# Optimization experiments

Hardware: AMD Instinct MI355X
Metric: run time of the kernel (lower is better)

## Reference

```python
import jax, jax.numpy as jnp
import numpy as np

# Config (matches BlockConfig defaults for linear attention)
B, S, D = 2, 4096, 2048
H, KVH, HD, CK = 16, 8, 128, 4   # n_heads, n_kv_heads, head_dim, conv_kernel
DQK, DV = KVH * HD, H * HD       # 1024, 2048
EPS = 1e-6


def setup_inputs() -> dict:
    key = jax.random.key(0)
    ks = jax.random.split(key, 12)
    std = 0.02
    return {
        "x": jax.random.normal(ks[0], (B, S, D), jnp.float32),
        "wq": jax.random.normal(ks[1], (DQK, D), jnp.float32) * std,
        "wk": jax.random.normal(ks[2], (DQK, D), jnp.float32) * std,
        "wv": jax.random.normal(ks[3], (DV, D), jnp.float32) * std,
        "wo": jax.random.normal(ks[4], (D, DV), jnp.float32) * std,
        "q_conv_w": jax.random.normal(ks[5], (DQK, 1, CK), jnp.float32) * std,
        "k_conv_w": jax.random.normal(ks[6], (DQK, 1, CK), jnp.float32) * std,
        "alpha_w": jax.random.normal(ks[7], (H, D), jnp.float32) * std,
        "alpha_b": jnp.zeros((H,), jnp.float32),
        "beta_w": jax.random.normal(ks[8], (H, D), jnp.float32) * std,
        "beta_b": jnp.zeros((H,), jnp.float32),
        "g_w": jax.random.normal(ks[9], (DV, D), jnp.float32) * std,
        "norm_q_w": jnp.ones((HD,), jnp.float32),
        "norm_k_w": jnp.ones((HD,), jnp.float32),
    }


def _rmsnorm(x, w):
    # normalize over last dim (head_dim) in fp32, elementwise affine, no bias
    xf = x.astype(jnp.float32)
    var = jnp.mean(xf * xf, axis=-1, keepdims=True)
    return (w * xf * jax.lax.rsqrt(var + EPS)).astype(x.dtype)


def _causal_dwconv(x, w):
    # x: (B, S, C); w: (C, 1, k) depthwise; torch Conv1d padding=k-1 then [:S]
    # == left-pad (k-1, 0) cross-correlation
    y = jax.lax.conv_general_dilated(
        x.transpose(0, 2, 1), w, window_strides=(1,),
        padding=[(CK - 1, 0)], feature_group_count=w.shape[0],
        dimension_numbers=("NCH", "OIH", "NCH"))
    return y.transpose(0, 2, 1)


def reference(x, wq, wk, wv, wo, q_conv_w, k_conv_w,
              alpha_w, alpha_b, beta_w, beta_b, g_w, norm_q_w, norm_k_w):
    Q = x @ wq.T                              # (B,S,DQK)
    K = x @ wk.T                              # (B,S,DQK)
    V = x @ wv.T                              # (B,S,DV)
    Q = _causal_dwconv(Q, q_conv_w)
    K = _causal_dwconv(K, k_conv_w)
    Q = _rmsnorm(Q.reshape(B, S, KVH, HD), norm_q_w)
    K = _rmsnorm(K.reshape(B, S, KVH, HD), norm_k_w)
    V = V.reshape(B, S, H, HD)
    alpha = jax.nn.sigmoid(x @ alpha_w.T + alpha_b)              # (B,S,H)
    beta = jax.nn.sigmoid(x @ beta_w.T + beta_b) / (HD ** 0.5)   # (B,S,H)
    rep = H // KVH
    Q = jnp.repeat(Q, rep, axis=2)            # (B,S,H,HD)
    K = jnp.repeat(K, rep, axis=2)

    # time-major for scan
    Qt = Q.transpose(1, 0, 2, 3)
    Kt = K.transpose(1, 0, 2, 3)
    Vt = V.transpose(1, 0, 2, 3)
    at = alpha.transpose(1, 0, 2)
    bt = beta.transpose(1, 0, 2)

    S0 = jnp.zeros((B, H, HD, HD), x.dtype)

    def step(S_state, inp):
        q_t, k_t, v_t, a_t, b_t = inp
        pred = jnp.einsum("bhd,bhdv->bhv", k_t, S_state)
        delta = v_t - pred
        update = jnp.einsum("bhv,bhd->bhdv", delta, k_t)
        S_state = a_t[:, :, None, None] * S_state + b_t[:, :, None, None] * update
        o_t = jnp.einsum("bhd,bhdv->bhv", q_t, S_state)
        return S_state, o_t

    _, O = jax.lax.scan(step, S0, (Qt, Kt, Vt, at, bt))  # O: (S,B,H,HD)
    out = O.transpose(1, 0, 2, 3).reshape(B, S, DV)
    g = jax.nn.sigmoid(x @ g_w.T)
    return (g * out) @ wo.T
```

## Files before the change

### kernel.cpp

```cpp
#include <hip/hip_runtime.h>
#include <stdint.h>

#define DEV static __device__ __forceinline__

typedef __bf16 bf16x8 __attribute__((ext_vector_type(8)));
typedef float f32x4 __attribute__((ext_vector_type(4)));

constexpr int Bc = 2, Sc = 4096, Dc = 2048, Hc = 16, KVHc = 8, HDc = 128;
constexpr int DQKc = 1024, DVc = 2048;
constexpr int Mc = Bc * Sc;
constexpr int NCATc = 6144;
constexpr int CT = 64;
constexpr int NCH = Sc / CT;
constexpr int COEF_STRIDE = 16896;
constexpr float EPSc = 1e-6f;

DEV uint16_t f2bf(float f) {
  uint32_t u = __float_as_uint(f);
  u += 0x7FFFu + ((u >> 16) & 1u);
  return (uint16_t)(u >> 16);
}
DEV float bf2f(uint16_t h) { return __uint_as_float(((uint32_t)h) << 16); }
DEV float sigmoidf_(float z) { return 1.0f / (1.0f + __expf(-z)); }

DEV void gload16(void* lds, const void* g) {
  auto gp = (const __attribute__((address_space(1))) uint32_t*)(uintptr_t)g;
  auto lp = (__attribute__((address_space(3))) uint32_t*)(uint32_t)(uintptr_t)lds;
  __builtin_amdgcn_global_load_lds(gp, lp, 16, 0, 0);
}

__global__ __launch_bounds__(256) void cast_kernel(const float* __restrict__ src,
                                                   uint16_t* __restrict__ dst, int n4) {
  int i = blockIdx.x * blockDim.x + threadIdx.x;
  int stride = gridDim.x * blockDim.x;
  for (; i < n4; i += stride) {
    float4 v = *(const float4*)(src + (size_t)i * 4);
    ushort4 o;
    o.x = f2bf(v.x); o.y = f2bf(v.y); o.z = f2bf(v.z); o.w = f2bf(v.w);
    *(ushort4*)(dst + (size_t)i * 4) = o;
  }
}

template <typename OutT>
__global__ __launch_bounds__(512, 2) void gemm256_bt(const uint16_t* __restrict__ A,
                                                     const uint16_t* __restrict__ Bw,
                                                     OutT* __restrict__ C, int Ndim, int Kdim,
                                                     int lda) {
  __shared__ uint16_t sT[2][2][2][8192];

  const int nbn = Ndim / 256;
  const int nwg = gridDim.x;
  int q = nwg >> 3, r = nwg & 7;
  int xcd = blockIdx.x & 7, lin = blockIdx.x >> 3;
  int swz = (xcd < r ? xcd * (q + 1) : r * (q + 1) + (xcd - r) * q) + lin;
  const int bm = swz / nbn, bn = swz % nbn;

  const int tid = threadIdx.x;
  const int wid = tid >> 6, lane = tid & 63;
  const int wm = wid >> 2, wn = wid & 3;
  const int lr = lane & 15;
  const int sswz8 = (((lane >> 4) ^ ((lr >> 1) & 3)) * 8);
  const int arow_base = wm * 128 + lr;
  const int brow_base = wn * 64 + lr;

  const uint16_t* Ab = A + (size_t)(bm * 256) * lda;
  const uint16_t* Bb = Bw + (size_t)(bn * 256) * Kdim;
  const int NT = Kdim >> 6;

  int srowA[2];
  int soff[2];
  const int wbase = tid & ~63;
#pragma unroll
  for (int u = 0; u < 2; ++u) {
    int L = u * 512 + tid;
    srowA[u] = L >> 2;
    soff[u] = (((L & 3) ^ ((L >> 3) & 3)) * 8);
  }

  auto STAGE = [&](int buf, int mat, int kh, int kt) {
    const uint16_t* gb = mat == 0 ? Ab : Bb;
    const int ld = mat == 0 ? lda : Kdim;
    uint16_t* rg = &sT[buf][mat][kh][0];
#pragma unroll
    for (int u = 0; u < 2; ++u) {
      const uint16_t* g = gb + (size_t)srowA[u] * ld + kt * 64 + kh * 32 + soff[u];
      gload16(rg + (u * 512 + wbase) * 8, g);
    }
  };

  f32x4 acc[8][4] = {};
  bf16x8 bfr[4];

  STAGE(0, 0, 0, 0); STAGE(0, 1, 0, 0);
  STAGE(0, 0, 1, 0); STAGE(0, 1, 1, 0);
  STAGE(1, 0, 0, 1); STAGE(1, 1, 0, 1);
  asm volatile("s_waitcnt vmcnt(4)" ::: "memory");
  __builtin_amdgcn_s_barrier();

  for (int kt = 0; kt < NT; ++kt) {
    const int buf = kt & 1;
    const uint16_t* aR0 = &sT[buf][0][0][0];
    const uint16_t* bR0 = &sT[buf][1][0][0];
    const uint16_t* aR1 = &sT[buf][0][1][0];
    const uint16_t* bR1 = &sT[buf][1][1][0];

    {
      bf16x8 af[4];
#pragma unroll
      for (int m = 0; m < 4; ++m)
        af[m] = *(const bf16x8*)&aR0[(arow_base + m * 16) * 32 + sswz8];
#pragma unroll
      for (int n = 0; n < 4; ++n)
        bfr[n] = *(const bf16x8*)&bR0[(brow_base + n * 16) * 32 + sswz8];
      if (kt + 1 < NT) STAGE(buf ^ 1, 0, 1, kt + 1);
      __builtin_amdgcn_s_setprio(1);
#pragma unroll
      for (int m = 0; m < 4; ++m)
#pragma unroll
        for (int n = 0; n < 4; ++n)
          acc[m][n] = __builtin_amdgcn_mfma_f32_16x16x32_bf16(af[m], bfr[n], acc[m][n], 0, 0, 0);
      __builtin_amdgcn_s_setprio(0);
      __builtin_amdgcn_s_barrier();
    }
    {
      bf16x8 af[4];
#pragma unroll
      for (int m = 0; m < 4; ++m)
        af[m] = *(const bf16x8*)&aR0[(arow_base + (m + 4) * 16) * 32 + sswz8];
      if (kt + 1 < NT) STAGE(buf ^ 1, 1, 1, kt + 1);
      __builtin_amdgcn_s_setprio(1);
#pragma unroll
      for (int m = 0; m < 4; ++m)
#pragma unroll
        for (int n = 0; n < 4; ++n)
          acc[m + 4][n] = __builtin_amdgcn_mfma_f32_16x16x32_bf16(af[m], bfr[n], acc[m + 4][n], 0, 0, 0);
      __builtin_amdgcn_s_setprio(0);
      __builtin_amdgcn_s_barrier();
    }
    {
      bf16x8 af[4];
#pragma unroll
      for (int m = 0; m < 4; ++m)
        af[m] = *(const bf16x8*)&aR1[(arow_base + m * 16) * 32 + sswz8];
#pragma unroll
      for (int n = 0; n < 4; ++n)
        bfr[n] = *(const bf16x8*)&bR1[(brow_base + n * 16) * 32 + sswz8];
      if (kt + 2 < NT) STAGE(buf, 0, 0, kt + 2);
      __builtin_amdgcn_s_setprio(1);
#pragma unroll
      for (int m = 0; m < 4; ++m)
#pragma unroll
        for (int n = 0; n < 4; ++n)
          acc[m][n] = __builtin_amdgcn_mfma_f32_16x16x32_bf16(af[m], bfr[n], acc[m][n], 0, 0, 0);
      __builtin_amdgcn_s_setprio(0);
      __builtin_amdgcn_s_barrier();
    }
    {
      bf16x8 af[4];
#pragma unroll
      for (int m = 0; m < 4; ++m)
        af[m] = *(const bf16x8*)&aR1[(arow_base + (m + 4) * 16) * 32 + sswz8];
      if (kt + 2 < NT) STAGE(buf, 1, 0, kt + 2);
      __builtin_amdgcn_s_setprio(1);
#pragma unroll
      for (int m = 0; m < 4; ++m)
#pragma unroll
        for (int n = 0; n < 4; ++n)
          acc[m + 4][n] = __builtin_amdgcn_mfma_f32_16x16x32_bf16(af[m], bfr[n], acc[m + 4][n], 0, 0, 0);
      __builtin_amdgcn_s_setprio(0);
    }
    if (kt + 1 < NT) {
      if (kt + 2 < NT)
        asm volatile("s_waitcnt vmcnt(4)" ::: "memory");
      else
        asm volatile("s_waitcnt vmcnt(0)" ::: "memory");
      __builtin_amdgcn_s_barrier();
    }
  }

  const int r0 = (lane >> 4) * 4;
#pragma unroll
  for (int m = 0; m < 8; ++m)
#pragma unroll
    for (int n = 0; n < 4; ++n) {
      int col = bn * 256 + wn * 64 + n * 16 + lr;
#pragma unroll
      for (int j = 0; j < 4; ++j) {
        int row = bm * 256 + wm * 128 + m * 16 + r0 + j;
        float val = acc[m][n][j];
        if constexpr (sizeof(OutT) == 2)
          C[(size_t)row * Ndim + col] = (OutT)f2bf(val);
        else
          C[(size_t)row * Ndim + col] = (OutT)val;
      }
    }
}

__global__ __launch_bounds__(256) void alphabeta_kernel(const float* __restrict__ x,
                                                        const float* __restrict__ aw,
                                                        const float* __restrict__ abias,
                                                        const float* __restrict__ bw,
                                                        const float* __restrict__ bbias,
                                                        float* __restrict__ out) {
  __shared__ float xs[4 * Dc];
  const int row0 = blockIdx.x * 4;
  const float* xp = x + (size_t)row0 * Dc;
  for (int i = threadIdx.x; i < 4 * Dc / 4; i += 256)
    *(float4*)&xs[i * 4] = *(const float4*)(xp + (size_t)i * 4);
  __syncthreads();
  const int o = threadIdx.x >> 3, lg = threadIdx.x & 7;
  const float* wrow = (o < 16) ? (aw + (size_t)o * Dc) : (bw + (size_t)(o - 16) * Dc);
  float s0 = 0.f, s1 = 0.f, s2 = 0.f, s3 = 0.f;
  for (int k = lg * 4; k < Dc; k += 32) {
    float4 wv = *(const float4*)(wrow + k);
    float4 x0 = *(const float4*)&xs[k];
    float4 x1 = *(const float4*)&xs[Dc + k];
    float4 x2 = *(const float4*)&xs[2 * Dc + k];
    float4 x3 = *(const float4*)&xs[3 * Dc + k];
    s0 += x0.x * wv.x + x0.y * wv.y + x0.z * wv.z + x0.w * wv.w;
    s1 += x1.x * wv.x + x1.y * wv.y + x1.z * wv.z + x1.w * wv.w;
    s2 += x2.x * wv.x + x2.y * wv.y + x2.z * wv.z + x2.w * wv.w;
    s3 += x3.x * wv.x + x3.y * wv.y + x3.z * wv.z + x3.w * wv.w;
  }
#pragma unroll
  for (int m = 1; m < 8; m <<= 1) {
    s0 += __shfl_xor(s0, m); s1 += __shfl_xor(s1, m);
    s2 += __shfl_xor(s2, m); s3 += __shfl_xor(s3, m);
  }
  if (lg == 0) {
    float bias = (o < 16) ? abias[o] : bbias[o - 16];
    float scale = (o >= 16) ? 0.08838834764831845f : 1.0f;
    out[(size_t)(row0 + 0) * 32 + o] = sigmoidf_(s0 + bias) * scale;
    out[(size_t)(row0 + 1) * 32 + o] = sigmoidf_(s1 + bias) * scale;
    out[(size_t)(row0 + 2) * 32 + o] = sigmoidf_(s2 + bias) * scale;
    out[(size_t)(row0 + 3) * 32 + o] = sigmoidf_(s3 + bias) * scale;
  }
}

__global__ __launch_bounds__(256) void convnorm_kernel(const uint16_t* __restrict__ C1,
                                                       const float* __restrict__ qcw,
                                                       const float* __restrict__ kcw,
                                                       const float* __restrict__ nqw,
                                                       const float* __restrict__ nkw,
                                                       uint16_t* __restrict__ Qn,
                                                       uint16_t* __restrict__ Kn) {
  const int wid = blockIdx.x * 4 + (threadIdx.x >> 6);
  const int lane = threadIdx.x & 63;
  const int kvh = wid & 7;
  const int t = (wid >> 3) & (Sc - 1);
  const int b = wid >> 15;
  float qv[2], kv[2];
#pragma unroll
  for (int half = 0; half < 2; ++half) {
    const int c = lane + half * 64;
    const int ch = kvh * HDc + c;
    float qs = 0.f, ks = 0.f;
#pragma unroll
    for (int j = 0; j < 4; ++j) {
      int tt = t - 3 + j;
      if (tt >= 0) {
        size_t rb = (size_t)(b * Sc + tt) * NCATc;
        qs = fmaf(bf2f(C1[rb + ch]), qcw[ch * 4 + j], qs);
        ks = fmaf(bf2f(C1[rb + 1024 + ch]), kcw[ch * 4 + j], ks);
      }
    }
    qv[half] = qs; kv[half] = ks;
  }
  float sq = qv[0] * qv[0] + qv[1] * qv[1];
  float sk = kv[0] * kv[0] + kv[1] * kv[1];
#pragma unroll
  for (int m = 1; m < 64; m <<= 1) { sq += __shfl_xor(sq, m); sk += __shfl_xor(sk, m); }
  const float rq = rsqrtf(sq * (1.f / HDc) + EPSc);
  const float rk = rsqrtf(sk * (1.f / HDc) + EPSc);
#pragma unroll
  for (int half = 0; half < 2; ++half) {
    const int c = lane + half * 64;
    size_t oidx = (size_t)(b * Sc + t) * DQKc + kvh * HDc + c;
    Qn[oidx] = f2bf(nqw[c] * qv[half] * rq);
    Kn[oidx] = f2bf(nkw[c] * kv[half] * rk);
  }
}

__global__ __launch_bounds__(256) void scores_kernel(const uint16_t* __restrict__ Qn,
                                                     const uint16_t* __restrict__ Kn,
                                                     const float* __restrict__ ab,
                                                     uint8_t* __restrict__ coef) {
  __shared__ __align__(16) char smem[109568];
  uint16_t* sK = (uint16_t*)smem;
  uint16_t* sQ = (uint16_t*)(smem + 17408);
  uint16_t* sM2 = (uint16_t*)smem;
  float* Lb = (float*)(smem + 108544);
  float* bbv = Lb + 128;

  auto Wt_p  = [&](int hd) { return (float*)(smem + hd * 17408); };
  auto Msh_p = [&](int hd) { return (uint16_t*)(smem + 34816 + hd * 18432); };
  auto Msl_p = [&](int hd) { return (uint16_t*)(smem + 44032 + hd * 18432); };
  auto Thh_p = [&](int hd) { return (uint16_t*)(smem + 71680 + hd * 18432); };
  auto Thl_p = [&](int hd) { return (uint16_t*)(smem + 80896 + hd * 18432); };

  const int bid = blockIdx.x;
  const int c = bid & 63, kh = (bid >> 6) & 7, b = bid >> 9;
  const int t0 = c * 64;
  const int tid = threadIdx.x;
  const int w = tid >> 6, l = tid & 63, lr = l & 15, lk = (l >> 4) * 8;
  const int sr = tid >> 2, sq2 = tid & 3;

  auto cb_p = [&](int hd) {
    return coef + (size_t)((b * Hc + kh * 2 + hd) * NCH + c) * COEF_STRIDE;
  };

  {
    const size_t rb = (size_t)(b * Sc + t0 + sr) * DQKc + kh * HDc + sq2 * 32;
#pragma unroll
    for (int u = 0; u < 4; ++u) {
      uint4 kv = *(const uint4*)(Kn + rb + u * 8);
      uint4 qv = *(const uint4*)(Qn + rb + u * 8);
      *(uint4*)&sK[sr * 136 + sq2 * 32 + u * 8] = kv;
      *(uint4*)&sQ[sr * 136 + sq2 * 32 + u * 8] = qv;
    }
  }
  if (tid < 128) {
    const int hd = tid >> 6, tt = tid & 63;
    const float* abp = ab + (size_t)(b * Sc + t0 + tt) * 32 + (kh * 2 + hd);
    float av = fmaxf(abp[0], 1e-30f);
    float bv = abp[16];
    float la = log2f(av);
    float L = la;
#pragma unroll
    for (int off = 1; off < 64; off <<= 1) {
      float up = __shfl_up(L, off, 64);
      if (tt >= off) L += up;
    }
    Lb[hd * 64 + tt] = L; bbv[hd * 64 + tt] = bv;
    float* gout = (float*)(cb_p(hd) + 16384);
    gout[tt] = exp2f(L - la);
    gout[64 + tt] = exp2f(L);
  }
  __syncthreads();

  f32x4 kkacc[4] = {}, qkacc[4] = {};
#pragma unroll
  for (int k0 = 0; k0 < 128; k0 += 32) {
    bf16x8 ka = *(const bf16x8*)&sK[(16 * w + lr) * 136 + k0 + lk];
    bf16x8 qa = *(const bf16x8*)&sQ[(16 * w + lr) * 136 + k0 + lk];
#pragma unroll
    for (int n = 0; n < 4; ++n) {
      bf16x8 kb = *(const bf16x8*)&sK[(16 * n + lr) * 136 + k0 + lk];
      kkacc[n] = __builtin_amdgcn_mfma_f32_16x16x32_bf16(ka, kb, kkacc[n], 0, 0, 0);
      qkacc[n] = __builtin_amdgcn_mfma_f32_16x16x32_bf16(qa, kb, qkacc[n], 0, 0, 0);
    }
  }
  __syncthreads();

#pragma unroll
  for (int hd = 0; hd < 2; ++hd) {
    float* Wt = Wt_p(hd);
    uint16_t* Mh = Msh_p(hd);
    uint16_t* Ml = Msl_p(hd);
    const float* Lh = Lb + hd * 64;
    const float* bh = bbv + hd * 64;
#pragma unroll
    for (int n = 0; n < 4; ++n)
#pragma unroll
      for (int jj = 0; jj < 4; ++jj) {
        const int i = 16 * w + (l >> 4) * 4 + jj;
        const int j = 16 * n + lr;
        float Li = Lh[i];
        float Lim = (i > 0) ? Lh[(i > 0) ? i - 1 : 0] : 0.f;
        float Lj = Lh[j];
        float bj = bh[j];
        float wv = (j < i) ? exp2f(Lim - Lj) * bj * kkacc[n][jj] : 0.f;
        Wt[j * 68 + i] = wv;
        float ms = (j <= i) ? exp2f(Li - Lj) * bj * qkacc[n][jj] : 0.f;
        uint16_t mh = f2bf(ms);
        Mh[i * 72 + j] = mh;
        Ml[i * 72 + j] = f2bf(ms - bf2f(mh));
      }
  }
  __syncthreads();

  if (tid < 128) {
    const int hd = tid >> 6, col = tid & 63;
    float* Wt = Wt_p(hd);
    uint16_t* Th = Thh_p(hd);
    uint16_t* Tl = Thl_p(hd);
    float acc[64];
#pragma unroll
    for (int i = 0; i < 64; ++i) acc[i] = 0.f;
#pragma unroll
    for (int ll = 0; ll < 64; ++ll) {
      float xl = ((col == ll) ? 1.f : 0.f) - acc[ll];
      uint16_t xh = f2bf(xl);
      Th[col * 72 + ll] = xh;
      Tl[col * 72 + ll] = f2bf(xl - bf2f(xh));
#pragma unroll
      for (int i = ll + 1; i < 64; ++i)
        acc[i] = fmaf(Wt[ll * 68 + i], xl, acc[i]);
    }
  }
  __syncthreads();

  for (int hd = 0; hd < 2; ++hd) {
    uint16_t* Mh = Msh_p(hd);
    uint16_t* Ml = Msl_p(hd);
    uint16_t* Th = Thh_p(hd);
    uint16_t* Tl = Thl_p(hd);
    uint16_t* m2out = (uint16_t*)cb_p(hd);
    uint16_t* eout = (uint16_t*)(cb_p(hd) + 8192);
    const float* Lh = Lb + hd * 64;
    const float* bh = bbv + hd * 64;
    const float L63 = Lh[63];

    {
      const int i2 = tid >> 2, tq = tid & 3;
      float gC = exp2f(L63 - Lh[i2]) * bh[i2];
      uint32_t pk[8];
#pragma unroll
      for (int p = 0; p < 8; ++p) {
        int t1 = tq * 16 + p * 2;
        float e0 = gC * (bf2f(Th[(t1 + 0) * 72 + i2]) + bf2f(Tl[(t1 + 0) * 72 + i2]));
        float e1 = gC * (bf2f(Th[(t1 + 1) * 72 + i2]) + bf2f(Tl[(t1 + 1) * 72 + i2]));
        pk[p] = (uint32_t)f2bf(e0) | ((uint32_t)f2bf(e1) << 16);
      }
      *(uint4*)(eout + i2 * 64 + tq * 16) = make_uint4(pk[0], pk[1], pk[2], pk[3]);
      *(uint4*)(eout + i2 * 64 + tq * 16 + 8) = make_uint4(pk[4], pk[5], pk[6], pk[7]);
    }

    f32x4 m2acc[4] = {};
#pragma unroll
    for (int k0 = 0; k0 < 64; k0 += 32) {
      bf16x8 ah = *(const bf16x8*)&Mh[(16 * w + lr) * 72 + k0 + lk];
      bf16x8 al = *(const bf16x8*)&Ml[(16 * w + lr) * 72 + k0 + lk];
#pragma unroll
      for (int n = 0; n < 4; ++n) {
        bf16x8 bhf = *(const bf16x8*)&Th[(16 * n + lr) * 72 + k0 + lk];
        bf16x8 blf = *(const bf16x8*)&Tl[(16 * n + lr) * 72 + k0 + lk];
        m2acc[n] = __builtin_amdgcn_mfma_f32_16x16x32_bf16(ah, bhf, m2acc[n], 0, 0, 0);
        m2acc[n] = __builtin_amdgcn_mfma_f32_16x16x32_bf16(ah, blf, m2acc[n], 0, 0, 0);
        m2acc[n] = __builtin_amdgcn_mfma_f32_16x16x32_bf16(al, bhf, m2acc[n], 0, 0, 0);
      }
    }
#pragma unroll
    for (int n = 0; n < 4; ++n)
#pragma unroll
      for (int jj = 0; jj < 4; ++jj) {
        const int i = 16 * w + (l >> 4) * 4 + jj;
        const int j = 16 * n + lr;
        sM2[i * 72 + j] = f2bf(m2acc[n][jj]);
      }
    __syncthreads();
    {
      const int i2 = tid >> 2, tq = tid & 3;
      uint4 a0 = *(const uint4*)&sM2[i2 * 72 + tq * 16];
      uint4 a1 = *(const uint4*)&sM2[i2 * 72 + tq * 16 + 8];
      *(uint4*)(m2out + i2 * 64 + tq * 16) = a0;
      *(uint4*)(m2out + i2 * 64 + tq * 16 + 8) = a1;
    }
    __syncthreads();
  }
}

__global__ __launch_bounds__(256) void scan_kernel(const uint16_t* __restrict__ Qn,
                                                   const uint16_t* __restrict__ Kn,
                                                   uint16_t* C1,
                                                   const uint8_t* __restrict__ coef) {
  __shared__ __align__(16) uint16_t Kb[64 * 136];
  __shared__ __align__(16) uint16_t Qb[64 * 136];
  __shared__ __align__(16) uint16_t Ktb[2][128 * 72];
  __shared__ __align__(16) uint16_t M2b[64 * 72];
  __shared__ __align__(16) uint16_t Eb[64 * 72];
  __shared__ __align__(16) uint16_t Vb[64 * 24];
  __shared__ __align__(16) uint16_t Rt[16 * 72];
  __shared__ __align__(16) uint16_t D2t[16 * 72];
  __shared__ __align__(16) uint16_t Sh[16 * 136];
  __shared__ __align__(16) uint16_t Slo[16 * 136];
  __shared__ float gABb[128];

  const int bid = blockIdx.x;
  const int kh = bid & 7;
  const int j2 = bid >> 3;
  const int sl = j2 >> 2;
  const int b = (j2 >> 1) & 1;
  const int h = kh * 2 + (j2 & 1);
  const int ch0 = (b * Hc + h) * NCH;

  const int tid = threadIdx.x;
  const int w = tid >> 6, l = tid & 63;
  const int lr = l & 15, lk = (l >> 4) * 8;
  const int row0 = 16 * w + (l >> 4) * 4;
  const int vcol = lr;
  const int sr = tid >> 2, sq2 = tid & 3;

  const size_t kqbase = (size_t)(b * Sc) * DQKc + kh * HDc;
  const size_t vbase = (size_t)(b * Sc) * NCATc + 2048 + h * HDc + sl * 16;
  uint16_t* Gb = C1 + (size_t)(b * Sc) * NCATc + 4096 + h * HDc + sl * 16 + vcol;

  float sreg[2][4] = {};
  uint4 kA[4], kB[4], qA[4], qB[4];
  ushort4 gv0, gv1;

  auto LOADS = [&](int cn, uint4 (&kd)[4], uint4 (&qd)[4], uint4 (&m2d)[2], uint4 (&ed)[2],
                   uint4& vd, float& gd, ushort4& gvd) {
    const size_t rb = kqbase + (size_t)(cn * CT + sr) * DQKc + sq2 * 32;
#pragma unroll
    for (int u = 0; u < 4; ++u) {
      kd[u] = *(const uint4*)(Kn + rb + u * 8);
      qd[u] = *(const uint4*)(Qn + rb + u * 8);
    }
    const uint16_t* cf = (const uint16_t*)(coef + (size_t)(ch0 + cn) * COEF_STRIDE);
#pragma unroll
    for (int e = 0; e < 2; ++e) {
      m2d[e] = *(const uint4*)(cf + sr * 64 + sq2 * 16 + e * 8);
      ed[e] = *(const uint4*)(cf + 4096 + sr * 64 + sq2 * 16 + e * 8);
    }
    if (tid < 128) {
      vd = *(const uint4*)(C1 + vbase + (size_t)(cn * CT + (tid >> 1)) * NCATc + (tid & 1) * 8);
      gd = ((const float*)(cf + 8192))[tid];
    }
    const uint16_t* gpre = Gb + (size_t)(cn * CT) * NCATc;
    gvd.x = gpre[(size_t)(row0 + 0) * NCATc];
    gvd.y = gpre[(size_t)(row0 + 1) * NCATc];
    gvd.z = gpre[(size_t)(row0 + 2) * NCATc];
    gvd.w = gpre[(size_t)(row0 + 3) * NCATc];
  };
  auto WSTAGE = [&](const uint4 (&kd)[4], const uint4 (&qd)[4], const uint4 (&m2d)[2],
                    const uint4 (&ed)[2], const uint4& vd, const float& gd) {
#pragma unroll
    for (int u = 0; u < 4; ++u) {
      *(uint4*)&Kb[sr * 136 + sq2 * 32 + u * 8] = kd[u];
      *(uint4*)&Qb[sr * 136 + sq2 * 32 + u * 8] = qd[u];
    }
#pragma unroll
    for (int e = 0; e < 2; ++e) {
      *(uint4*)&M2b[sr * 72 + sq2 * 16 + e * 8] = m2d[e];
      *(uint4*)&Eb[sr * 72 + sq2 * 16 + e * 8] = ed[e];
    }
    if (tid < 128) {
      *(uint4*)&Vb[(tid >> 1) * 24 + (tid & 1) * 8] = vd;
      gABb[tid] = gd;
    }
  };
  auto SCAT = [&](uint16_t* Kt, const uint4 (&kd)[4], int u) {
    const int c0 = sq2 * 32 + u * 8;
    const int tsw = sr ^ (sq2 << 4);
    uint32_t x0 = kd[u].x, x1 = kd[u].y, x2 = kd[u].z, x3 = kd[u].w;
    Kt[(c0 + 0) * 72 + tsw] = (uint16_t)x0; Kt[(c0 + 1) * 72 + tsw] = (uint16_t)(x0 >> 16);
    Kt[(c0 + 2) * 72 + tsw] = (uint16_t)x1; Kt[(c0 + 3) * 72 + tsw] = (uint16_t)(x1 >> 16);
    Kt[(c0 + 4) * 72 + tsw] = (uint16_t)x2; Kt[(c0 + 5) * 72 + tsw] = (uint16_t)(x2 >> 16);
    Kt[(c0 + 6) * 72 + tsw] = (uint16_t)x3; Kt[(c0 + 7) * 72 + tsw] = (uint16_t)(x3 >> 16);
  };

  auto CHUNK = [&](int c, bool pre, uint4 (&kcur)[4], uint4 (&knxt)[4],
                   uint4 (&qcur)[4], uint4 (&qnxt)[4], ushort4& gvcur, ushort4& gvnxt) {
    uint4 m2d[2], ed[2]; uint4 vd; float gd = 0.f;
    if (pre) LOADS(c + 1, knxt, qnxt, m2d, ed, vd, gd, gvnxt);
    const uint16_t* Ktc = Ktb[c & 1];
    uint16_t* Ktn = Ktb[(c + 1) & 1];

    f32x4 accP = {0, 0, 0, 0}, accPq = {0, 0, 0, 0};
#pragma unroll
    for (int k0 = 0; k0 < 128; k0 += 32) {
      bf16x8 ka = *(const bf16x8*)&Kb[(16 * w + lr) * 136 + k0 + lk];
      bf16x8 qa = *(const bf16x8*)&Qb[(16 * w + lr) * 136 + k0 + lk];
      bf16x8 shf = *(const bf16x8*)&Sh[lr * 136 + k0 + lk];
      bf16x8 slf = *(const bf16x8*)&Slo[lr * 136 + k0 + lk];
      accP = __builtin_amdgcn_mfma_f32_16x16x32_bf16(ka, shf, accP, 0, 0, 0);
      accP = __builtin_amdgcn_mfma_f32_16x16x32_bf16(ka, slf, accP, 0, 0, 0);
      accPq = __builtin_amdgcn_mfma_f32_16x16x32_bf16(qa, shf, accPq, 0, 0, 0);
      accPq = __builtin_amdgcn_mfma_f32_16x16x32_bf16(qa, slf, accPq, 0, 0, 0);
    }
    {
      float rv[4];
#pragma unroll
      for (int j = 0; j < 4; ++j) {
        float vv = bf2f(Vb[(row0 + j) * 24 + vcol]);
        float ga = gABb[row0 + j];
        rv[j] = vv - ga * accP[j];
      }
      uint32_t r01 = (uint32_t)f2bf(rv[0]) | ((uint32_t)f2bf(rv[1]) << 16);
      uint32_t r23 = (uint32_t)f2bf(rv[2]) | ((uint32_t)f2bf(rv[3]) << 16);
      *(uint2*)&Rt[vcol * 72 + row0] = make_uint2(r01, r23);
    }
    __syncthreads();

    f32x4 accD2 = {0, 0, 0, 0}, accO = {0, 0, 0, 0};
#pragma unroll
    for (int k0 = 0; k0 < 64; k0 += 32) {
      bf16x8 rb8 = *(const bf16x8*)&Rt[lr * 72 + k0 + lk];
      bf16x8 ea = *(const bf16x8*)&Eb[(16 * w + lr) * 72 + k0 + lk];
      bf16x8 ma = *(const bf16x8*)&M2b[(16 * w + lr) * 72 + k0 + lk];
      accD2 = __builtin_amdgcn_mfma_f32_16x16x32_bf16(ea, rb8, accD2, 0, 0, 0);
      accO = __builtin_amdgcn_mfma_f32_16x16x32_bf16(ma, rb8, accO, 0, 0, 0);
    }
    if (pre) { SCAT(Ktn, knxt, 0); SCAT(Ktn, knxt, 1); }
    {
      uint16_t* gp = Gb + (size_t)(c * CT) * NCATc;
      uint16_t gvv[4] = {gvcur.x, gvcur.y, gvcur.z, gvcur.w};
#pragma unroll
      for (int j = 0; j < 4; ++j) {
        float o = gABb[64 + row0 + j] * accPq[j] + accO[j];
        float gg = sigmoidf_(bf2f(gvv[j]));
        gp[(size_t)(row0 + j) * NCATc] = f2bf(o * gg);
      }
      uint32_t d01 = (uint32_t)f2bf(accD2[0]) | ((uint32_t)f2bf(accD2[1]) << 16);
      uint32_t d23 = (uint32_t)f2bf(accD2[2]) | ((uint32_t)f2bf(accD2[3]) << 16);
      *(uint2*)&D2t[vcol * 72 + row0] = make_uint2(d01, d23);
    }
    __syncthreads();

    const float gT = gABb[127];
    f32x4 accY[2] = {{0, 0, 0, 0}, {0, 0, 0, 0}};
#pragma unroll
    for (int k0 = 0; k0 < 64; k0 += 32) {
      const int ksw = (k0 + lk) ^ (w << 4);
      bf16x8 db = *(const bf16x8*)&D2t[lr * 72 + k0 + lk];
      bf16x8 ka0 = *(const bf16x8*)&Ktc[(32 * w + lr) * 72 + ksw];
      bf16x8 ka1 = *(const bf16x8*)&Ktc[(32 * w + 16 + lr) * 72 + ksw];
      accY[0] = __builtin_amdgcn_mfma_f32_16x16x32_bf16(ka0, db, accY[0], 0, 0, 0);
      accY[1] = __builtin_amdgcn_mfma_f32_16x16x32_bf16(ka1, db, accY[1], 0, 0, 0);
    }
    if (pre) { SCAT(Ktn, knxt, 2); SCAT(Ktn, knxt, 3); }
#pragma unroll
    for (int m = 0; m < 2; ++m) {
      uint16_t hi[4], lo[4];
#pragma unroll
      for (int j = 0; j < 4; ++j) {
        float s = gT * sreg[m][j] + accY[m][j];
        sreg[m][j] = s;
        hi[j] = f2bf(s);
        lo[j] = f2bf(s - bf2f(hi[j]));
      }
      const int dk0 = 32 * w + m * 16 + (l >> 4) * 4;
      *(uint2*)&Sh[vcol * 136 + dk0] =
          make_uint2((uint32_t)hi[0] | ((uint32_t)hi[1] << 16),
                     (uint32_t)hi[2] | ((uint32_t)hi[3] << 16));
      *(uint2*)&Slo[vcol * 136 + dk0] =
          make_uint2((uint32_t)lo[0] | ((uint32_t)lo[1] << 16),
                     (uint32_t)lo[2] | ((uint32_t)lo[3] << 16));
    }
    if (pre) WSTAGE(knxt, qnxt, m2d, ed, vd, gd);
    __syncthreads();
  };

  {
    uint4 m2d[2], ed[2]; uint4 vd; float gd = 0.f;
    LOADS(0, kA, qA, m2d, ed, vd, gd, gv0);
    WSTAGE(kA, qA, m2d, ed, vd, gd);
#pragma unroll
    for (int u = 0; u < 4; ++u) SCAT(Ktb[0], kA, u);
  }
  for (int i = tid; i < 16 * 136; i += 256) { Sh[i] = 0; Slo[i] = 0; }
  __syncthreads();

  for (int c2 = 0; c2 < NCH; c2 += 2) {
    CHUNK(c2, true, kA, kB, qA, qB, gv0, gv1);
    CHUNK(c2 + 1, c2 + 2 < NCH, kB, kA, qB, qA, gv1, gv0);
  }
}

extern "C" void kernel_launch(void* const* d_in, const int* in_sizes, int n_in,
                              void* d_out, int out_size, void* d_ws, size_t ws_size,
                              hipStream_t stream) {
  (void)in_sizes; (void)n_in; (void)out_size; (void)ws_size;
  const float* x     = (const float*)d_in[0];
  const float* wq    = (const float*)d_in[1];
  const float* wk    = (const float*)d_in[2];
  const float* wv    = (const float*)d_in[3];
  const float* wo    = (const float*)d_in[4];
  const float* qcw   = (const float*)d_in[5];
  const float* kcw   = (const float*)d_in[6];
  const float* aw    = (const float*)d_in[7];
  const float* abias = (const float*)d_in[8];
  const float* bw    = (const float*)d_in[9];
  const float* bbias = (const float*)d_in[10];
  const float* gw    = (const float*)d_in[11];
  const float* nqw   = (const float*)d_in[12];
  const float* nkw   = (const float*)d_in[13];

  uint8_t* ws = (uint8_t*)d_ws;
  uint16_t* xb   = (uint16_t*)(ws);
  uint16_t* wcat = (uint16_t*)(ws + 33554432);
  uint16_t* wob  = (uint16_t*)(ws + 58720256);
  uint16_t* c1   = (uint16_t*)(ws + 67108864);
  float*    abuf = (float*)   (ws + 167772160);
  uint16_t* qn   = (uint16_t*)(ws + 168820736);
  uint16_t* kn   = (uint16_t*)(ws + 185597952);
  uint8_t*  cofs = (uint8_t*)ws;

  cast_kernel<<<2048, 256, 0, stream>>>(x, xb, Mc * Dc / 4);
  cast_kernel<<<1024, 256, 0, stream>>>(wq, wcat, DQKc * Dc / 4);
  cast_kernel<<<1024, 256, 0, stream>>>(wk, wcat + DQKc * Dc, DQKc * Dc / 4);
  cast_kernel<<<1024, 256, 0, stream>>>(wv, wcat + 2 * DQKc * Dc, DVc * Dc / 4);
  cast_kernel<<<1024, 256, 0, stream>>>(gw, wcat + 2 * DQKc * Dc + DVc * Dc, DVc * Dc / 4);
  cast_kernel<<<1024, 256, 0, stream>>>(wo, wob, DVc * Dc / 4);

  gemm256_bt<uint16_t><<<768, 512, 0, stream>>>(xb, wcat, c1, NCATc, Dc, Dc);
  alphabeta_kernel<<<2048, 256, 0, stream>>>(x, aw, abias, bw, bbias, abuf);
  convnorm_kernel<<<16384, 256, 0, stream>>>(c1, qcw, kcw, nqw, nkw, qn, kn);
  scores_kernel<<<1024, 256, 0, stream>>>(qn, kn, abuf, cofs);
  scan_kernel<<<256, 256, 0, stream>>>(qn, kn, c1, cofs);
  gemm256_bt<float><<<256, 512, 0, stream>>>(c1 + 4096, wob, (float*)d_out, DVc, Dc, NCATc);
}
```

Before: 699.0 us.

## Precompute K^T·E per chunk in scores kernel to shorten the serial scan

The scores kernel now forms the product of the transposed chunk keys with the gated E matrix (a 128x64 F matrix) and writes it to the coefficient buffer, replacing E. The scan kernel then updates its state directly with F·R in the same MFMA pass as the output, removing one sync, the D2 staging and the per-chunk K transpose scatter. Q/K fragments, alpha/beta gates, V and the gate input are held in registers rather than LDS, and the scan kernel is given an occupancy hint of 3 blocks per CU. This moves work off the sequential critical path but increases coefficient traffic and LDS use in the scores kernel, and F is rounded to bf16 before use.

```diff
diff --git a/kernel.cpp b/kernel.cpp
--- a/kernel.cpp
+++ b/kernel.cpp
@@ -12,7 +12,7 @@
 constexpr int NCATc = 6144;
 constexpr int CT = 64;
 constexpr int NCH = Sc / CT;
-constexpr int COEF_STRIDE = 16896;
+constexpr int COEF_STRIDE = 25088;
 constexpr float EPSc = 1e-6f;
 
 DEV uint16_t f2bf(float f) {
@@ -285,12 +285,16 @@
                                                      const uint16_t* __restrict__ Kn,
                                                      const float* __restrict__ ab,
                                                      uint8_t* __restrict__ coef) {
-  __shared__ __align__(16) char smem[109568];
+  __shared__ __align__(16) char smem[137728];
   uint16_t* sK = (uint16_t*)smem;
   uint16_t* sQ = (uint16_t*)(smem + 17408);
-  uint16_t* sM2 = (uint16_t*)smem;
+  uint16_t* sF = (uint16_t*)smem;
+  uint16_t* sM2 = (uint16_t*)(smem + 18432);
   float* Lb = (float*)(smem + 108544);
   float* bbv = Lb + 128;
+  uint16_t* Ktg = (uint16_t*)(smem + 109568);
+  uint16_t* Et = (uint16_t*)(smem + 128000);
+  float* gCb = (float*)(smem + 137216);
 
   auto Wt_p  = [&](int hd) { return (float*)(smem + hd * 17408); };
   auto Msh_p = [&](int hd) { return (uint16_t*)(smem + 34816 + hd * 18432); };
@@ -332,7 +336,7 @@
       if (tt >= off) L += up;
     }
     Lb[hd * 64 + tt] = L; bbv[hd * 64 + tt] = bv;
-    float* gout = (float*)(cb_p(hd) + 16384);
+    float* gout = (float*)(cb_p(hd) + 24576);
     gout[tt] = exp2f(L - la);
     gout[64 + tt] = exp2f(L);
   }
@@ -348,6 +352,25 @@
       bf16x8 kb = *(const bf16x8*)&sK[(16 * n + lr) * 136 + k0 + lk];
       kkacc[n] = __builtin_amdgcn_mfma_f32_16x16x32_bf16(ka, kb, kkacc[n], 0, 0, 0);
       qkacc[n] = __builtin_amdgcn_mfma_f32_16x16x32_bf16(qa, kb, qkacc[n], 0, 0, 0);
+    }
+  }
+  __syncthreads();
+
+  {
+#pragma unroll
+    for (int u = 0; u < 4; ++u) {
+      uint4 kd = *(const uint4*)&sK[sr * 136 + sq2 * 32 + u * 8];
+      const int c0 = sq2 * 32 + u * 8;
+      const int tsw = sr ^ (sq2 << 4);
+      uint32_t x0 = kd.x, x1 = kd.y, x2 = kd.z, x3 = kd.w;
+      Ktg[(c0 + 0) * 72 + tsw] = (uint16_t)x0; Ktg[(c0 + 1) * 72 + tsw] = (uint16_t)(x0 >> 16);
+      Ktg[(c0 + 2) * 72 + tsw] = (uint16_t)x1; Ktg[(c0 + 3) * 72 + tsw] = (uint16_t)(x1 >> 16);
+      Ktg[(c0 + 4) * 72 + tsw] = (uint16_t)x2; Ktg[(c0 + 5) * 72 + tsw] = (uint16_t)(x2 >> 16);
+      Ktg[(c0 + 6) * 72 + tsw] = (uint16_t)x3; Ktg[(c0 + 7) * 72 + tsw] = (uint16_t)(x3 >> 16);
+    }
+    if (tid < 128) {
+      const int hd = tid >> 6, tt = tid & 63;
+      gCb[hd * 64 + tt] = exp2f(Lb[hd * 64 + 63] - Lb[hd * 64 + tt]) * bbv[hd * 64 + tt];
     }
   }
   __syncthreads();
@@ -406,25 +429,18 @@
     uint16_t* Th = Thh_p(hd);
     uint16_t* Tl = Thl_p(hd);
     uint16_t* m2out = (uint16_t*)cb_p(hd);
-    uint16_t* eout = (uint16_t*)(cb_p(hd) + 8192);
-    const float* Lh = Lb + hd * 64;
-    const float* bh = bbv + hd * 64;
-    const float L63 = Lh[63];
-
-    {
-      const int i2 = tid >> 2, tq = tid & 3;
-      float gC = exp2f(L63 - Lh[i2]) * bh[i2];
-      uint32_t pk[8];
-#pragma unroll
-      for (int p = 0; p < 8; ++p) {
-        int t1 = tq * 16 + p * 2;
-        float e0 = gC * (bf2f(Th[(t1 + 0) * 72 + i2]) + bf2f(Tl[(t1 + 0) * 72 + i2]));
-        float e1 = gC * (bf2f(Th[(t1 + 1) * 72 + i2]) + bf2f(Tl[(t1 + 1) * 72 + i2]));
-        pk[p] = (uint32_t)f2bf(e0) | ((uint32_t)f2bf(e1) << 16);
-      }
-      *(uint4*)(eout + i2 * 64 + tq * 16) = make_uint4(pk[0], pk[1], pk[2], pk[3]);
-      *(uint4*)(eout + i2 * 64 + tq * 16 + 8) = make_uint4(pk[4], pk[5], pk[6], pk[7]);
-    }
+    uint16_t* fout = (uint16_t*)cb_p(hd) + 4096;
+
+    {
+      const int j2 = tid >> 2, tq = tid & 3;
+#pragma unroll
+      for (int p = 0; p < 16; ++p) {
+        int t1 = tq * 16 + p;
+        float ev = gCb[hd * 64 + t1] * (bf2f(Th[j2 * 72 + t1]) + bf2f(Tl[j2 * 72 + t1]));
+        Et[j2 * 72 + t1] = f2bf(ev);
+      }
+    }
+    __syncthreads();
 
     f32x4 m2acc[4] = {};
 #pragma unroll
@@ -440,6 +456,22 @@
         m2acc[n] = __builtin_amdgcn_mfma_f32_16x16x32_bf16(al, bhf, m2acc[n], 0, 0, 0);
       }
     }
+    f32x4 facc[2][4] = {};
+#pragma unroll
+    for (int k0 = 0; k0 < 64; k0 += 32) {
+      bf16x8 eb[4];
+#pragma unroll
+      for (int n = 0; n < 4; ++n)
+        eb[n] = *(const bf16x8*)&Et[(16 * n + lr) * 72 + k0 + lk];
+      const int ksw = (k0 + lk) ^ (w << 4);
+      bf16x8 ka0 = *(const bf16x8*)&Ktg[(32 * w + lr) * 72 + ksw];
+      bf16x8 ka1 = *(const bf16x8*)&Ktg[(32 * w + 16 + lr) * 72 + ksw];
+#pragma unroll
+      for (int n = 0; n < 4; ++n) {
+        facc[0][n] = __builtin_amdgcn_mfma_f32_16x16x32_bf16(ka0, eb[n], facc[0][n], 0, 0, 0);
+        facc[1][n] = __builtin_amdgcn_mfma_f32_16x16x32_bf16(ka1, eb[n], facc[1][n], 0, 0, 0);
+      }
+    }
 #pragma unroll
     for (int n = 0; n < 4; ++n)
 #pragma unroll
@@ -447,6 +479,8 @@
         const int i = 16 * w + (l >> 4) * 4 + jj;
         const int j = 16 * n + lr;
         sM2[i * 72 + j] = f2bf(m2acc[n][jj]);
+        sF[(32 * w + (l >> 4) * 4 + jj) * 72 + j] = f2bf(facc[0][n][jj]);
+        sF[(32 * w + 16 + (l >> 4) * 4 + jj) * 72 + j] = f2bf(facc[1][n][jj]);
       }
     __syncthreads();
     {
@@ -455,26 +489,32 @@
       uint4 a1 = *(const uint4*)&sM2[i2 * 72 + tq * 16 + 8];
       *(uint4*)(m2out + i2 * 64 + tq * 16) = a0;
       *(uint4*)(m2out + i2 * 64 + tq * 16 + 8) = a1;
+#pragma unroll
+      for (int e = 0; e < 4; ++e) {
+        int L = tid * 4 + e;
+        int rw = L >> 3, cu = (L & 7) * 8;
+        *(uint4*)(fout + rw * 64 + cu) = *(const uint4*)&sF[rw * 72 + cu];
+      }
     }
     __syncthreads();
   }
 }
 
-__global__ __launch_bounds__(256) void scan_kernel(const uint16_t* __restrict__ Qn,
-                                                   const uint16_t* __restrict__ Kn,
-                                                   uint16_t* C1,
-                                                   const uint8_t* __restrict__ coef) {
-  __shared__ __align__(16) uint16_t Kb[64 * 136];
-  __shared__ __align__(16) uint16_t Qb[64 * 136];
-  __shared__ __align__(16) uint16_t Ktb[2][128 * 72];
+struct ChSt {
+  uint4 k[4], q[4];
+  float ga[4], gb[4], gT;
+  uint16_t v[4], gv[4];
+};
+
+__global__ __launch_bounds__(256, 3) void scan_kernel(const uint16_t* __restrict__ Qn,
+                                                      const uint16_t* __restrict__ Kn,
+                                                      uint16_t* C1,
+                                                      const uint8_t* __restrict__ coef) {
   __shared__ __align__(16) uint16_t M2b[64 * 72];
-  __shared__ __align__(16) uint16_t Eb[64 * 72];
-  __shared__ __align__(16) uint16_t Vb[64 * 24];
+  __shared__ __align__(16) uint16_t Fb[128 * 72];
   __shared__ __align__(16) uint16_t Rt[16 * 72];
-  __shared__ __align__(16) uint16_t D2t[16 * 72];
   __shared__ __align__(16) uint16_t Sh[16 * 136];
   __shared__ __align__(16) uint16_t Slo[16 * 136];
-  __shared__ float gABb[128];
 
   const int bid = blockIdx.x;
   const int kh = bid & 7;
@@ -492,78 +532,59 @@
   const int sr = tid >> 2, sq2 = tid & 3;
 
   const size_t kqbase = (size_t)(b * Sc) * DQKc + kh * HDc;
-  const size_t vbase = (size_t)(b * Sc) * NCATc + 2048 + h * HDc + sl * 16;
+  const size_t vbase = (size_t)(b * Sc) * NCATc + 2048 + h * HDc + sl * 16 + vcol;
   uint16_t* Gb = C1 + (size_t)(b * Sc) * NCATc + 4096 + h * HDc + sl * 16 + vcol;
 
   float sreg[2][4] = {};
-  uint4 kA[4], kB[4], qA[4], qB[4];
-  ushort4 gv0, gv1;
-
-  auto LOADS = [&](int cn, uint4 (&kd)[4], uint4 (&qd)[4], uint4 (&m2d)[2], uint4 (&ed)[2],
-                   uint4& vd, float& gd, ushort4& gvd) {
-    const size_t rb = kqbase + (size_t)(cn * CT + sr) * DQKc + sq2 * 32;
+
+  auto LOADS = [&](int cn, ChSt& st, uint4 (&m2d)[2], uint4 (&fd)[4]) {
+    const size_t krow = kqbase + (size_t)(cn * CT + 16 * w + lr) * DQKc + lk;
 #pragma unroll
     for (int u = 0; u < 4; ++u) {
-      kd[u] = *(const uint4*)(Kn + rb + u * 8);
-      qd[u] = *(const uint4*)(Qn + rb + u * 8);
+      st.k[u] = *(const uint4*)(Kn + krow + u * 32);
+      st.q[u] = *(const uint4*)(Qn + krow + u * 32);
     }
     const uint16_t* cf = (const uint16_t*)(coef + (size_t)(ch0 + cn) * COEF_STRIDE);
 #pragma unroll
-    for (int e = 0; e < 2; ++e) {
+    for (int e = 0; e < 2; ++e)
       m2d[e] = *(const uint4*)(cf + sr * 64 + sq2 * 16 + e * 8);
-      ed[e] = *(const uint4*)(cf + 4096 + sr * 64 + sq2 * 16 + e * 8);
-    }
-    if (tid < 128) {
-      vd = *(const uint4*)(C1 + vbase + (size_t)(cn * CT + (tid >> 1)) * NCATc + (tid & 1) * 8);
-      gd = ((const float*)(cf + 8192))[tid];
-    }
-    const uint16_t* gpre = Gb + (size_t)(cn * CT) * NCATc;
-    gvd.x = gpre[(size_t)(row0 + 0) * NCATc];
-    gvd.y = gpre[(size_t)(row0 + 1) * NCATc];
-    gvd.z = gpre[(size_t)(row0 + 2) * NCATc];
-    gvd.w = gpre[(size_t)(row0 + 3) * NCATc];
+#pragma unroll
+    for (int e = 0; e < 4; ++e)
+      fd[e] = *(const uint4*)(cf + 4096 + (tid * 4 + e) * 8);
+    const float* gf = (const float*)(cf + 12288);
+    float4 ga4 = *(const float4*)(gf + row0);
+    float4 gb4 = *(const float4*)(gf + 64 + row0);
+    st.ga[0] = ga4.x; st.ga[1] = ga4.y; st.ga[2] = ga4.z; st.ga[3] = ga4.w;
+    st.gb[0] = gb4.x; st.gb[1] = gb4.y; st.gb[2] = gb4.z; st.gb[3] = gb4.w;
+    st.gT = gf[127];
+#pragma unroll
+    for (int j = 0; j < 4; ++j) {
+      st.v[j] = C1[vbase + (size_t)(cn * CT + row0 + j) * NCATc];
+      st.gv[j] = Gb[(size_t)(cn * CT + row0 + j) * NCATc];
+    }
   };
-  auto WSTAGE = [&](const uint4 (&kd)[4], const uint4 (&qd)[4], const uint4 (&m2d)[2],
-                    const uint4 (&ed)[2], const uint4& vd, const float& gd) {
+  auto WSTAGE = [&](const uint4 (&m2d)[2], const uint4 (&fd)[4]) {
+#pragma unroll
+    for (int e = 0; e < 2; ++e)
+      *(uint4*)&M2b[sr * 72 + sq2 * 16 + e * 8] = m2d[e];
+#pragma unroll
+    for (int e = 0; e < 4; ++e) {
+      int L = tid * 4 + e;
+      *(uint4*)&Fb[(L >> 3) * 72 + (L & 7) * 8] = fd[e];
+    }
+  };
+
+  auto CHUNK = [&](int c, bool pre, ChSt& cur, ChSt& nxt) {
+    uint4 m2d[2]; uint4 fd[4];
+    if (pre) LOADS(c + 1, nxt, m2d, fd);
+
+    f32x4 accP = {0, 0, 0, 0}, accPq = {0, 0, 0, 0};
 #pragma unroll
     for (int u = 0; u < 4; ++u) {
-      *(uint4*)&Kb[sr * 136 + sq2 * 32 + u * 8] = kd[u];
-      *(uint4*)&Qb[sr * 136 + sq2 * 32 + u * 8] = qd[u];
-    }
-#pragma unroll
-    for (int e = 0; e < 2; ++e) {
-      *(uint4*)&M2b[sr * 72 + sq2 * 16 + e * 8] = m2d[e];
-      *(uint4*)&Eb[sr * 72 + sq2 * 16 + e * 8] = ed[e];
-    }
-    if (tid < 128) {
-      *(uint4*)&Vb[(tid >> 1) * 24 + (tid & 1) * 8] = vd;
-      gABb[tid] = gd;
-    }
-  };
-  auto SCAT = [&](uint16_t* Kt, const uint4 (&kd)[4], int u) {
-    const int c0 = sq2 * 32 + u * 8;
-    const int tsw = sr ^ (sq2 << 4);
-    uint32_t x0 = kd[u].x, x1 = kd[u].y, x2 = kd[u].z, x3 = kd[u].w;
-    Kt[(c0 + 0) * 72 + tsw] = (uint16_t)x0; Kt[(c0 + 1) * 72 + tsw] = (uint16_t)(x0 >> 16);
-    Kt[(c0 + 2) * 72 + tsw] = (uint16_t)x1; Kt[(c0 + 3) * 72 + tsw] = (uint16_t)(x1 >> 16);
-    Kt[(c0 + 4) * 72 + tsw] = (uint16_t)x2; Kt[(c0 + 5) * 72 + tsw] = (uint16_t)(x2 >> 16);
-    Kt[(c0 + 6) * 72 + tsw] = (uint16_t)x3; Kt[(c0 + 7) * 72 + tsw] = (uint16_t)(x3 >> 16);
-  };
-
-  auto CHUNK = [&](int c, bool pre, uint4 (&kcur)[4], uint4 (&knxt)[4],
-                   uint4 (&qcur)[4], uint4 (&qnxt)[4], ushort4& gvcur, ushort4& gvnxt) {
-    uint4 m2d[2], ed[2]; uint4 vd; float gd = 0.f;
-    if (pre) LOADS(c + 1, knxt, qnxt, m2d, ed, vd, gd, gvnxt);
-    const uint16_t* Ktc = Ktb[c & 1];
-    uint16_t* Ktn = Ktb[(c + 1) & 1];
-
-    f32x4 accP = {0, 0, 0, 0}, accPq = {0, 0, 0, 0};
-#pragma unroll
-    for (int k0 = 0; k0 < 128; k0 += 32) {
-      bf16x8 ka = *(const bf16x8*)&Kb[(16 * w + lr) * 136 + k0 + lk];
-      bf16x8 qa = *(const bf16x8*)&Qb[(16 * w + lr) * 136 + k0 + lk];
-      bf16x8 shf = *(const bf16x8*)&Sh[lr * 136 + k0 + lk];
-      bf16x8 slf = *(const bf16x8*)&Slo[lr * 136 + k0 + lk];
+      bf16x8 shf = *(const bf16x8*)&Sh[lr * 136 + u * 32 + lk];
+      bf16x8 slf = *(const bf16x8*)&Slo[lr * 136 + u * 32 + lk];
+      bf16x8 ka = *(const bf16x8*)&cur.k[u];
+      bf16x8 qa = *(const bf16x8*)&cur.q[u];
       accP = __builtin_amdgcn_mfma_f32_16x16x32_bf16(ka, shf, accP, 0, 0, 0);
       accP = __builtin_amdgcn_mfma_f32_16x16x32_bf16(ka, slf, accP, 0, 0, 0);
       accPq = __builtin_amdgcn_mfma_f32_16x16x32_bf16(qa, shf, accPq, 0, 0, 0);
@@ -572,65 +593,45 @@
     {
       float rv[4];
 #pragma unroll
-      for (int j = 0; j < 4; ++j) {
-        float vv = bf2f(Vb[(row0 + j) * 24 + vcol]);
-        float ga = gABb[row0 + j];
-        rv[j] = vv - ga * accP[j];
-      }
+      for (int j = 0; j < 4; ++j)
+        rv[j] = bf2f(cur.v[j]) - cur.ga[j] * accP[j];
       uint32_t r01 = (uint32_t)f2bf(rv[0]) | ((uint32_t)f2bf(rv[1]) << 16);
       uint32_t r23 = (uint32_t)f2bf(rv[2]) | ((uint32_t)f2bf(rv[3]) << 16);
       *(uint2*)&Rt[vcol * 72 + row0] = make_uint2(r01, r23);
     }
     __syncthreads();
 
-    f32x4 accD2 = {0, 0, 0, 0}, accO = {0, 0, 0, 0};
+    f32x4 accO = {0, 0, 0, 0};
+    f32x4 accY0 = {0, 0, 0, 0}, accY1 = {0, 0, 0, 0};
 #pragma unroll
     for (int k0 = 0; k0 < 64; k0 += 32) {
       bf16x8 rb8 = *(const bf16x8*)&Rt[lr * 72 + k0 + lk];
-      bf16x8 ea = *(const bf16x8*)&Eb[(16 * w + lr) * 72 + k0 + lk];
       bf16x8 ma = *(const bf16x8*)&M2b[(16 * w + lr) * 72 + k0 + lk];
-      accD2 = __builtin_amdgcn_mfma_f32_16x16x32_bf16(ea, rb8, accD2, 0, 0, 0);
+      bf16x8 f0 = *(const bf16x8*)&Fb[(32 * w + lr) * 72 + k0 + lk];
+      bf16x8 f1 = *(const bf16x8*)&Fb[(32 * w + 16 + lr) * 72 + k0 + lk];
       accO = __builtin_amdgcn_mfma_f32_16x16x32_bf16(ma, rb8, accO, 0, 0, 0);
-    }
-    if (pre) { SCAT(Ktn, knxt, 0); SCAT(Ktn, knxt, 1); }
+      accY0 = __builtin_amdgcn_mfma_f32_16x16x32_bf16(f0, rb8, accY0, 0, 0, 0);
+      accY1 = __builtin_amdgcn_mfma_f32_16x16x32_bf16(f1, rb8, accY1, 0, 0, 0);
+    }
     {
       uint16_t* gp = Gb + (size_t)(c * CT) * NCATc;
-      uint16_t gvv[4] = {gvcur.x, gvcur.y, gvcur.z, gvcur.w};
 #pragma unroll
       for (int j = 0; j < 4; ++j) {
-        float o = gABb[64 + row0 + j] * accPq[j] + accO[j];
-        float gg = sigmoidf_(bf2f(gvv[j]));
+        float o = cur.gb[j] * accPq[j] + accO[j];
+        float gg = sigmoidf_(bf2f(cur.gv[j]));
         gp[(size_t)(row0 + j) * NCATc] = f2bf(o * gg);
       }
-      uint32_t d01 = (uint32_t)f2bf(accD2[0]) | ((uint32_t)f2bf(accD2[1]) << 16);
-      uint32_t d23 = (uint32_t)f2bf(accD2[2]) | ((uint32_t)f2bf(accD2[3]) << 16);
-      *(uint2*)&D2t[vcol * 72 + row0] = make_uint2(d01, d23);
-    }
-    __syncthreads();
-
-    const float gT = gABb[127];
-    f32x4 accY[2] = {{0, 0, 0, 0}, {0, 0, 0, 0}};
-#pragma unroll
-    for (int k0 = 0; k0 < 64; k0 += 32) {
-      const int ksw = (k0 + lk) ^ (w << 4);
-      bf16x8 db = *(const bf16x8*)&D2t[lr * 72 + k0 + lk];
-      bf16x8 ka0 = *(const bf16x8*)&Ktc[(32 * w + lr) * 72 + ksw];
-      bf16x8 ka1 = *(const bf16x8*)&Ktc[(32 * w + 16 + lr) * 72 + ksw];
-      accY[0] = __builtin_amdgcn_mfma_f32_16x16x32_bf16(ka0, db, accY[0], 0, 0, 0);
-      accY[1] = __builtin_amdgcn_mfma_f32_16x16x32_bf16(ka1, db, accY[1], 0, 0, 0);
-    }
-    if (pre) { SCAT(Ktn, knxt, 2); SCAT(Ktn, knxt, 3); }
-#pragma unroll
-    for (int m = 0; m < 2; ++m) {
+    }
+    {
       uint16_t hi[4], lo[4];
 #pragma unroll
       for (int j = 0; j < 4; ++j) {
-        float s = gT * sreg[m][j] + accY[m][j];
-        sreg[m][j] = s;
+        float s = cur.gT * sreg[0][j] + accY0[j];
+        sreg[0][j] = s;
         hi[j] = f2bf(s);
         lo[j] = f2bf(s - bf2f(hi[j]));
       }
-      const int dk0 = 32 * w + m * 16 + (l >> 4) * 4;
+      const int dk0 = 32 * w + (l >> 4) * 4;
       *(uint2*)&Sh[vcol * 136 + dk0] =
           make_uint2((uint32_t)hi[0] | ((uint32_t)hi[1] << 16),
                      (uint32_t)hi[2] | ((uint32_t)hi[3] << 16));
@@ -638,23 +639,40 @@
           make_uint2((uint32_t)lo[0] | ((uint32_t)lo[1] << 16),
                      (uint32_t)lo[2] | ((uint32_t)lo[3] << 16));
     }
-    if (pre) WSTAGE(knxt, qnxt, m2d, ed, vd, gd);
+    {
+      uint16_t hi[4], lo[4];
+#pragma unroll
+      for (int j = 0; j < 4; ++j) {
+        float s = cur.gT * sreg[1][j] + accY1[j];
+        sreg[1][j] = s;
+        hi[j] = f2bf(s);
+        lo[j] = f2bf(s - bf2f(hi[j]));
+      }
+      const int dk0 = 32 * w + 16 + (l >> 4) * 4;
+      *(uint2*)&Sh[vcol * 136 + dk0] =
+          make_uint2((uint32_t)hi[0] | ((uint32_t)hi[1] << 16),
+                     (uint32_t)hi[2] | ((uint32_t)hi[3] << 16));
+      *(uint2*)&Slo[vcol * 136 + dk0] =
+          make_uint2((uint32_t)lo[0] | ((uint32_t)lo[1] << 16),
+                     (uint32_t)lo[2] | ((uint32_t)lo[3] << 16));
+    }
     __syncthreads();
+
+    if (pre) WSTAGE(m2d, fd);
   };
 
+  ChSt sA, sB;
   {
-    uint4 m2d[2], ed[2]; uint4 vd; float gd = 0.f;
-    LOADS(0, kA, qA, m2d, ed, vd, gd, gv0);
-    WSTAGE(kA, qA, m2d, ed, vd, gd);
-#pragma unroll
-    for (int u = 0; u < 4; ++u) SCAT(Ktb[0], kA, u);
+    uint4 m2d[2]; uint4 fd[4];
+    LOADS(0, sA, m2d, fd);
+    WSTAGE(m2d, fd);
   }
   for (int i = tid; i < 16 * 136; i += 256) { Sh[i] = 0; Slo[i] = 0; }
   __syncthreads();
 
   for (int c2 = 0; c2 < NCH; c2 += 2) {
-    CHUNK(c2, true, kA, kB, qA, qB, gv0, gv1);
-    CHUNK(c2 + 1, c2 + 2 < NCH, kB, kA, qB, qA, gv1, gv0);
+    CHUNK(c2, true, sA, sB);
+    CHUNK(c2 + 1, c2 + 2 < NCH, sB, sA);
   }
 }
 
```

Result: slower. 887.4 us (+26.9%).
